# Kernel tuning notes

Hardware: AMD Instinct MI355X
Metric: run time of the kernel (lower is better)

Reference implementation:

```python
import jax, jax.numpy as jnp
import numpy as np

N_TARGETS = 4
BATCH_SIZE = 4
B = N_TARGETS * BATCH_SIZE
N_SAMPLES = 1024
LAYERS = [(128, 128), (256, 64), (512, 32)]  # (channels, spatial)
EPS_COS = 1e-10


def setup_inputs() -> dict:
    key = jax.random.key(0)
    inp = {}
    for l, (c, s) in enumerate(LAYERS):
        k1, k2, k3, k4, key = jax.random.split(key, 5)
        n = s * s
        inp[f't{l}'] = jax.random.normal(k1, (N_TARGETS, c, s, s), dtype=jnp.float32)
        inp[f'g{l}'] = jax.random.normal(k2, (B, c, s, s), dtype=jnp.float32)
        inp[f'ix{l}'] = jax.random.randint(k3, (B, N_SAMPLES), 0, n)
        inp[f'iy{l}'] = jax.random.randint(k4, (B, N_SAMPLES), 0, n)
    return inp


def _cos_remd(x, y):
    # x: (b,n,c), y: (b,m,c)
    xn = jnp.linalg.norm(x, axis=2, keepdims=True)            # (b,n,1)
    yn = jnp.linalg.norm(y, axis=2, keepdims=True)            # (b,m,1)
    cross = jnp.einsum('bnc,bmc->bnm', x, y)                  # (b,n,m)
    dist = 1.0 - cross / (xn * yn.transpose(0, 2, 1) + EPS_COS)
    m1 = dist.min(axis=1).mean(axis=1)                        # min over n, mean over m
    m2 = dist.min(axis=2).mean(axis=1)                        # min over m, mean over n
    return jnp.maximum(m1, m2)                                # (b,)


def _moment_loss(x, y):
    mu_x = x.mean(axis=1, keepdims=True)
    mu_y = y.mean(axis=1, keepdims=True)
    mu_diff = jnp.abs(mu_x - mu_y).mean(axis=(1, 2))
    x_c = x - mu_x
    y_c = y - mu_y
    x_cov = jnp.einsum('bnc,bnd->bcd', x_c, x_c) / (x.shape[1] - 1)
    y_cov = jnp.einsum('bmc,bmd->bcd', y_c, y_c) / (y.shape[1] - 1)
    cov_diff = jnp.abs(x_cov - y_cov).mean(axis=(1, 2))
    return mu_diff + cov_diff                                 # (b,)


def _layer_loss(t, g, ix, iy):
    b, c, h, w = g.shape
    y = jnp.tile(t, (BATCH_SIZE, 1, 1, 1)).reshape(b, t.shape[1], -1)  # (b,c,n_y)
    x = g.reshape(b, c, -1)                                            # (b,c,n_x)
    x = jnp.take_along_axis(x, ix[:, None, :], axis=2)                 # (b,c,ns)
    y = jnp.take_along_axis(y, iy[:, None, :], axis=2)                 # (b,c,ns)
    x = x.transpose(0, 2, 1)
    y = y.transpose(0, 2, 1)
    return _cos_remd(x, y) + _moment_loss(x, y)


def reference(t0, g0, t1, g1, t2, g2, ix0, iy0, ix1, iy1, ix2, iy2):
    loss = (_layer_loss(t0, g0, ix0, iy0)
            + _layer_loss(t1, g1, ix1, iy1)
            + _layer_loss(t2, g2, ix2, iy2))
    return loss.reshape(BATCH_SIZE, N_TARGETS).mean(axis=0)   # (n_targets,)
```

## Files before the change

### kernel.cpp

```cpp
#include <hip/hip_runtime.h>
#include <math.h>

#define NT 4
#define BSZ 4
#define BB 16
#define NS 1024
#define CHF 1024
#define MAXL 3

typedef unsigned short u16;
typedef __attribute__((ext_vector_type(8))) short bf16x8;
typedef __attribute__((ext_vector_type(4))) float f32x4;

struct LayerP {
    const float *g, *t;
    const int *ix, *iy;
    u16 *Xt, *Yt, *Xs, *Ys;
    float *xp, *yp;
    float *psx, *psy;
    float *rxn, *ryn;
    float *sx, *sy;
    unsigned *m1u, *m2u;
    float *cov;
    int C, n, nchunk, ntri, lid, hs, csl, xblk, yblk;
};
struct Tab {
    LayerP L[MAXL];
    int nl, nb, b0, ysh;
    float* losspart;
};

__device__ __forceinline__ unsigned fenc(float f) {
    unsigned u = __float_as_uint(f);
    return (u & 0x80000000u) ? ~u : (u | 0x80000000u);
}
__device__ __forceinline__ float fdec(unsigned u) {
    unsigned v = (u & 0x80000000u) ? (u & 0x7FFFFFFFu) : ~u;
    return __uint_as_float(v);
}
__device__ __forceinline__ u16 f2bf(float f) {
    unsigned u = __float_as_uint(f);
    unsigned r = u + 0x7FFFu + ((u >> 16) & 1u);
    return (u16)(r >> 16);
}
__device__ __forceinline__ float bf2f(u16 h) {
    return __uint_as_float((unsigned)h << 16);
}

__device__ __forceinline__ void gload16(const float* src, float* dst) {
    __builtin_amdgcn_global_load_lds(
        (const __attribute__((address_space(1))) float*)src,
        (__attribute__((address_space(3))) float*)dst, 16, 0, 0);
}
__device__ __forceinline__ void wait_rem(int rem) {
    if (rem >= 3)      asm volatile("s_waitcnt vmcnt(3)" ::: "memory");
    else if (rem == 2) asm volatile("s_waitcnt vmcnt(2)" ::: "memory");
    else if (rem == 1) asm volatile("s_waitcnt vmcnt(1)" ::: "memory");
    else               asm volatile("s_waitcnt vmcnt(0)" ::: "memory");
}

__global__ __launch_bounds__(256) void gather(Tab tab)
{
    int f = blockIdx.x;
    int l = 0, side = 0, c = 0, grp = 0, h = 0;
    #pragma unroll
    for (int li = 0; li < MAXL; ++li) {
        if (li >= tab.nl) break;
        if (f < tab.L[li].xblk) { l = li; side = 0; goto decoded; }
        f -= tab.L[li].xblk;
        if (f < tab.L[li].yblk) { l = li; side = 1; goto decoded; }
        f -= tab.L[li].yblk;
    }
decoded:;
    const LayerP P = tab.L[l];
    c = f % P.C; f /= P.C;
    int ytg = (tab.ysh == NT) ? NT : tab.nb;
    int gdim = side ? ytg : tab.nb;
    grp = f % gdim; h = f / gdim;

    int tid = threadIdx.x;
    int wv = tid >> 6, lane = tid & 63;
    int csl = P.csl;
    int sbase = h * csl * CHF;
    __shared__ __align__(16) float buf[4][CHF];
    __shared__ float red[4][4];

    if (side == 0) {
        int bl = grp, bg = tab.b0 + bl;
        const float* __restrict__ grow = P.g + ((size_t)bg * P.C + c) * P.n;
        const int* __restrict__ ixr = P.ix + bg * NS;
        int px[4];
        #pragma unroll
        for (int r = 0; r < 4; ++r) px[r] = ixr[tid + r * 256] - sbase;
        __builtin_amdgcn_sched_barrier(0);
        for (int d = 0; d < csl; ++d)
            gload16(grow + sbase + d * CHF + wv * 256 + lane * 4, &buf[d][wv * 256]);
        float xv[4] = {0.f, 0.f, 0.f, 0.f};
        for (int ch = 0; ch < csl; ++ch) {
            wait_rem(csl - 1 - ch);
            __builtin_amdgcn_s_barrier();
            __builtin_amdgcn_sched_barrier(0);
            #pragma unroll
            for (int r = 0; r < 4; ++r) {
                int rel = px[r] - ch * CHF;
                if ((unsigned)rel < (unsigned)CHF) xv[r] = buf[ch][rel];
            }
        }
        u16* __restrict__ xo = P.Xt + ((size_t)bl * P.C + c) * NS;
        float ax = 0.f;
        #pragma unroll
        for (int r = 0; r < 4; ++r) {
            if ((unsigned)px[r] < (unsigned)(csl * CHF)) {
                u16 hb = f2bf(xv[r]);
                xo[tid + r * 256] = hb;
                ax += bf2f(hb);
            }
        }
        for (int o = 32; o > 0; o >>= 1) ax += __shfl_down(ax, o);
        if (lane == 0) red[0][wv] = ax;
        __syncthreads();
        if (tid == 0)
            P.psx[((size_t)h * tab.nb + bl) * P.C + c] =
                red[0][0] + red[0][1] + red[0][2] + red[0][3];
    } else {
        int nk, tgt, bls[4];
        if (tab.ysh == NT) {
            nk = 4; tgt = grp;
            #pragma unroll
            for (int k = 0; k < 4; ++k) bls[k] = tgt + NT * k;
        } else {
            nk = 1; bls[0] = grp; tgt = (tab.b0 + grp) % NT;
            bls[1] = bls[2] = bls[3] = 0;
        }
        const float* __restrict__ trow = P.t + ((size_t)tgt * P.C + c) * P.n;
        int py[4][4];
        #pragma unroll
        for (int k = 0; k < 4; ++k)
            if (k < nk) {
                const int* iyr = P.iy + (tab.b0 + bls[k]) * NS;
                #pragma unroll
                for (int r = 0; r < 4; ++r) py[k][r] = iyr[tid + r * 256] - sbase;
            }
        __builtin_amdgcn_sched_barrier(0);
        for (int d = 0; d < csl; ++d)
            gload16(trow + sbase + d * CHF + wv * 256 + lane * 4, &buf[d][wv * 256]);
        float yv[4][4];
        #pragma unroll
        for (int k = 0; k < 4; ++k)
            #pragma unroll
            for (int r = 0; r < 4; ++r) yv[k][r] = 0.f;
        for (int ch = 0; ch < csl; ++ch) {
            wait_rem(csl - 1 - ch);
            __builtin_amdgcn_s_barrier();
            __builtin_amdgcn_sched_barrier(0);
            #pragma unroll
            for (int k = 0; k < 4; ++k)
                if (k < nk) {
                    #pragma unroll
                    for (int r = 0; r < 4; ++r) {
                        int rel = py[k][r] - ch * CHF;
                        if ((unsigned)rel < (unsigned)CHF) yv[k][r] = buf[ch][rel];
                    }
                }
        }
        #pragma unroll
        for (int k = 0; k < 4; ++k) {
            if (k >= nk) break;
            u16* __restrict__ yo = P.Yt + ((size_t)bls[k] * P.C + c) * NS;
            float ay = 0.f;
            #pragma unroll
            for (int r = 0; r < 4; ++r) {
                if ((unsigned)py[k][r] < (unsigned)(csl * CHF)) {
                    u16 hb = f2bf(yv[k][r]);
                    yo[tid + r * 256] = hb;
                    ay += bf2f(hb);
                }
            }
            for (int o = 32; o > 0; o >>= 1) ay += __shfl_down(ay, o);
            if (lane == 0) red[k][wv] = ay;
        }
        __syncthreads();
        if (tid < nk)
            P.psy[((size_t)h * tab.nb + bls[tid]) * P.C + c] =
                red[tid][0] + red[tid][1] + red[tid][2] + red[tid][3];
    }
}

__global__ void transpose_k(Tab tab)
{
    int x = blockIdx.x, l = 0;
    while (l < MAXL - 1 && x >= tab.L[l].C / 64) { x -= tab.L[l].C / 64; ++l; }
    const LayerP P = tab.L[l];
    int z = blockIdx.z;
    int bl = z >> 1, which = z & 1;
    const u16* __restrict__ Zt = which ? P.Yt : P.Xt;
    u16* __restrict__ Zs = which ? P.Ys : P.Xs;
    float* __restrict__ zp = which ? P.yp : P.xp;
    int C = P.C;
    int ctile = x;
    int c0 = ctile * 64, s0 = blockIdx.y * 64;
    __shared__ __align__(16) u16 T[64][72];
    int tid = threadIdx.x;
    #pragma unroll
    for (int rep = 0; rep < 2; ++rep) {
        int q = tid + rep * 256;
        int rr = q >> 3, seg = q & 7;
        *(float4*)&T[rr][seg * 8] =
            *(const float4*)&Zt[((size_t)bl * C + c0 + rr) * NS + s0 + seg * 8];
    }
    __syncthreads();
    #pragma unroll
    for (int rep = 0; rep < 2; ++rep) {
        int q = tid + rep * 256;
        int sr = q >> 3, cs = q & 7;
        __align__(16) u16 tmp[8];
        float p = 0.f;
        #pragma unroll
        for (int e = 0; e < 8; ++e) {
            u16 h = T[cs * 8 + e][sr];
            tmp[e] = h;
            float v = bf2f(h);
            p = fmaf(v, v, p);
        }
        *(float4*)&Zs[((size_t)bl * NS + s0 + sr) * C + c0 + cs * 8] = *(float4*)tmp;
        p += __shfl_xor(p, 1);
        p += __shfl_xor(p, 2);
        p += __shfl_xor(p, 4);
        if (cs == 0)
            zp[((size_t)bl * P.nchunk + ctile) * NS + s0 + sr] = p;
    }
}

__global__ void colnorm_reduce(Tab tab)
{
    const LayerP P = tab.L[blockIdx.y];
    int bl = blockIdx.z;
    int nb = tab.nb;
    int s = blockIdx.x * 256 + threadIdx.x;
    float ax = 0.f, ay = 0.f;
    for (int k = 0; k < P.nchunk; ++k) {
        size_t o = ((size_t)bl * P.nchunk + k) * NS + s;
        ax += P.xp[o];
        ay += P.yp[o];
    }
    P.rxn[bl * NS + s] = rsqrtf(ax);
    P.ryn[bl * NS + s] = rsqrtf(ay);
    P.m1u[bl * NS + s] = 0xFFFFFFFFu;
    P.m2u[bl * NS + s] = 0xFFFFFFFFu;
    int cq = P.C >> 2;
    for (int c = blockIdx.x * cq + threadIdx.x; c < (blockIdx.x + 1) * cq; c += 256) {
        float sx = 0.f, sy = 0.f;
        for (int h = 0; h < P.hs; ++h) {
            sx += P.psx[((size_t)h * nb + bl) * P.C + c];
            sy += P.psy[((size_t)h * nb + bl) * P.C + c];
        }
        P.sx[bl * P.C + c] = sx;
        P.sy[bl * P.C + c] = sy;
    }
}

__global__ __launch_bounds__(256) void cross_mfma(Tab tab)
{
    int z = blockIdx.z;
    int l = z / tab.nb, bl = z - l * tab.nb;
    const LayerP P = tab.L[l];
    int C = P.C;
    int i0 = blockIdx.x * 128, j0 = blockIdx.y * 128;
    __shared__ __align__(16) u16 As[128][40], Bs[128][40];
    int tid = threadIdx.x;
    int w = tid >> 6, lane = tid & 63;
    int wr = w >> 1, wc = w & 1;
    int q = lane >> 4, r = lane & 15;
    const u16* __restrict__ Xb = P.Xs + ((size_t)bl * NS + i0) * C;
    const u16* __restrict__ Yb = P.Ys + ((size_t)bl * NS + j0) * C;
    f32x4 acc[4][4];
    #pragma unroll
    for (int m = 0; m < 4; ++m)
        #pragma unroll
        for (int nn = 0; nn < 4; ++nn) acc[m][nn] = (f32x4){0.f, 0.f, 0.f, 0.f};

    for (int kk = 0; kk < C; kk += 32) {
        __syncthreads();
        #pragma unroll
        for (int rep = 0; rep < 2; ++rep) {
            int qid = tid + rep * 256;
            int row = qid >> 2, seg = qid & 3;
            size_t off = (size_t)row * C + kk + seg * 8;
            *(float4*)&As[row][seg * 8] = *(const float4*)&Xb[off];
            *(float4*)&Bs[row][seg * 8] = *(const float4*)&Yb[off];
        }
        __syncthreads();
        bf16x8 a[4], b[4];
        #pragma unroll
        for (int m = 0; m < 4; ++m)
            a[m] = *(const bf16x8*)&As[wr * 64 + m * 16 + r][q * 8];
        #pragma unroll
        for (int nn = 0; nn < 4; ++nn)
            b[nn] = *(const bf16x8*)&Bs[wc * 64 + nn * 16 + r][q * 8];
        #pragma unroll
        for (int m = 0; m < 4; ++m)
            #pragma unroll
            for (int nn = 0; nn < 4; ++nn)
                acc[m][nn] = __builtin_amdgcn_mfma_f32_16x16x32_bf16(a[m], b[nn], acc[m][nn], 0, 0, 0);
    }

    float rxl[4][4], ryl[4];
    #pragma unroll
    for (int m = 0; m < 4; ++m)
        #pragma unroll
        for (int reg = 0; reg < 4; ++reg)
            rxl[m][reg] = P.rxn[bl * NS + i0 + wr * 64 + m * 16 + q * 4 + reg];
    #pragma unroll
    for (int nn = 0; nn < 4; ++nn)
        ryl[nn] = P.ryn[bl * NS + j0 + wc * 64 + nn * 16 + r];

    float rm[4][4], cm[4];
    #pragma unroll
    for (int m = 0; m < 4; ++m)
        #pragma unroll
        for (int reg = 0; reg < 4; ++reg) rm[m][reg] = 1e30f;
    #pragma unroll
    for (int nn = 0; nn < 4; ++nn) cm[nn] = 1e30f;
    #pragma unroll
    for (int m = 0; m < 4; ++m)
        #pragma unroll
        for (int nn = 0; nn < 4; ++nn)
            #pragma unroll
            for (int reg = 0; reg < 4; ++reg) {
                float d = 1.f - acc[m][nn][reg] * rxl[m][reg] * ryl[nn];
                rm[m][reg] = fminf(rm[m][reg], d);
                cm[nn] = fminf(cm[nn], d);
            }
    #pragma unroll
    for (int m = 0; m < 4; ++m)
        #pragma unroll
        for (int reg = 0; reg < 4; ++reg) {
            float v = rm[m][reg];
            v = fminf(v, __shfl_xor(v, 1));
            v = fminf(v, __shfl_xor(v, 2));
            v = fminf(v, __shfl_xor(v, 4));
            v = fminf(v, __shfl_xor(v, 8));
            rm[m][reg] = v;
        }
    if (r == 0) {
        #pragma unroll
        for (int m = 0; m < 4; ++m)
            #pragma unroll
            for (int reg = 0; reg < 4; ++reg) {
                int i = i0 + wr * 64 + m * 16 + q * 4 + reg;
                atomicMin(&P.m2u[bl * NS + i], fenc(rm[m][reg]));
            }
    }
    #pragma unroll
    for (int nn = 0; nn < 4; ++nn) {
        float v = cm[nn];
        v = fminf(v, __shfl_xor(v, 16));
        v = fminf(v, __shfl_xor(v, 32));
        cm[nn] = v;
    }
    if (q == 0) {
        #pragma unroll
        for (int nn = 0; nn < 4; ++nn) {
            int j = j0 + wc * 64 + nn * 16 + r;
            atomicMin(&P.m1u[bl * NS + j], fenc(cm[nn]));
        }
    }
}

__global__ __launch_bounds__(256) void cov_mfma(Tab tab)
{
    int x = blockIdx.x, l = 0;
    while (l < MAXL - 1 && x >= tab.L[l].ntri) { x -= tab.L[l].ntri; ++l; }
    const LayerP P = tab.L[l];
    int u = x;
    int bl = blockIdx.y;
    int C = P.C;
    int ty = 0;
    while ((ty + 1) * (ty + 2) / 2 <= u) ++ty;
    int tx = u - ty * (ty + 1) / 2;
    int c0 = ty * 128, d0 = tx * 128;
    float wgt = (tx == ty) ? 1.f : 2.f;

    __shared__ __align__(16) u16 As[128][40], Bs[128][40], Cs2[128][40], Ds[128][40];
    int tid = threadIdx.x;
    int w = tid >> 6, lane = tid & 63;
    int wr = w >> 1, wc = w & 1;
    int q = lane >> 4, r = lane & 15;
    const u16* __restrict__ Xc = P.Xt + ((size_t)bl * C + c0) * NS;
    const u16* __restrict__ Xd = P.Xt + ((size_t)bl * C + d0) * NS;
    const u16* __restrict__ Yc = P.Yt + ((size_t)bl * C + c0) * NS;
    const u16* __restrict__ Yd = P.Yt + ((size_t)bl * C + d0) * NS;

    f32x4 accX[4][4], accY[4][4];
    #pragma unroll
    for (int m = 0; m < 4; ++m)
        #pragma unroll
        for (int nn = 0; nn < 4; ++nn) {
            accX[m][nn] = (f32x4){0.f, 0.f, 0.f, 0.f};
            accY[m][nn] = (f32x4){0.f, 0.f, 0.f, 0.f};
        }

    for (int ss = 0; ss < NS; ss += 32) {
        __syncthreads();
        #pragma unroll
        for (int rep = 0; rep < 2; ++rep) {
            int qid = tid + rep * 256;
            int row = qid >> 2, seg = qid & 3;
            size_t off = (size_t)row * NS + ss + seg * 8;
            *(float4*)&As[row][seg * 8]  = *(const float4*)&Xc[off];
            *(float4*)&Bs[row][seg * 8]  = *(const float4*)&Xd[off];
            *(float4*)&Cs2[row][seg * 8] = *(const float4*)&Yc[off];
            *(float4*)&Ds[row][seg * 8]  = *(const float4*)&Yd[off];
        }
        __syncthreads();
        {
            bf16x8 a[4], b[4];
            #pragma unroll
            for (int m = 0; m < 4; ++m) a[m] = *(const bf16x8*)&As[wr * 64 + m * 16 + r][q * 8];
            #pragma unroll
            for (int nn = 0; nn < 4; ++nn) b[nn] = *(const bf16x8*)&Bs[wc * 64 + nn * 16 + r][q * 8];
            #pragma unroll
            for (int m = 0; m < 4; ++m)
                #pragma unroll
                for (int nn = 0; nn < 4; ++nn)
                    accX[m][nn] = __builtin_amdgcn_mfma_f32_16x16x32_bf16(a[m], b[nn], accX[m][nn], 0, 0, 0);
        }
        {
            bf16x8 a[4], b[4];
            #pragma unroll
            for (int m = 0; m < 4; ++m) a[m] = *(const bf16x8*)&Cs2[wr * 64 + m * 16 + r][q * 8];
            #pragma unroll
            for (int nn = 0; nn < 4; ++nn) b[nn] = *(const bf16x8*)&Ds[wc * 64 + nn * 16 + r][q * 8];
            #pragma unroll
            for (int m = 0; m < 4; ++m)
                #pragma unroll
                for (int nn = 0; nn < 4; ++nn)
                    accY[m][nn] = __builtin_amdgcn_mfma_f32_16x16x32_bf16(a[m], b[nn], accY[m][nn], 0, 0, 0);
        }
    }

    float scxv[4][4], scyv[4][4], sdxv[4], sdyv[4];
    #pragma unroll
    for (int m = 0; m < 4; ++m)
        #pragma unroll
        for (int reg = 0; reg < 4; ++reg) {
            int c = c0 + wr * 64 + m * 16 + q * 4 + reg;
            scxv[m][reg] = P.sx[bl * C + c];
            scyv[m][reg] = P.sy[bl * C + c];
        }
    #pragma unroll
    for (int nn = 0; nn < 4; ++nn) {
        int d = d0 + wc * 64 + nn * 16 + r;
        sdxv[nn] = P.sx[bl * C + d];
        sdyv[nn] = P.sy[bl * C + d];
    }
    const float invNS = 1.f / NS, invNSm1 = 1.f / (NS - 1);
    float tsum = 0.f;
    #pragma unroll
    for (int m = 0; m < 4; ++m)
        #pragma unroll
        for (int nn = 0; nn < 4; ++nn)
            #pragma unroll
            for (int reg = 0; reg < 4; ++reg) {
                float cx = (accX[m][nn][reg] - scxv[m][reg] * sdxv[nn] * invNS) * invNSm1;
                float cy = (accY[m][nn][reg] - scyv[m][reg] * sdyv[nn] * invNS) * invNSm1;
                tsum += fabsf(cx - cy);
            }
    tsum *= wgt;
    __shared__ float redc[4];
    for (int o = 32; o > 0; o >>= 1) tsum += __shfl_down(tsum, o);
    if (lane == 0) redc[w] = tsum;
    __syncthreads();
    if (tid == 0)
        P.cov[(size_t)bl * P.ntri + u] = redc[0] + redc[1] + redc[2] + redc[3];
}

__global__ void finalize_kernel(Tab tab)
{
    const LayerP P = tab.L[blockIdx.x];
    int bl = blockIdx.y;
    int tid = threadIdx.x;
    int C = P.C;
    float s1 = 0.f, s2 = 0.f, smu = 0.f, scov = 0.f;
    for (int s = tid; s < NS; s += 256) {
        s1 += fdec(P.m1u[bl * NS + s]);
        s2 += fdec(P.m2u[bl * NS + s]);
    }
    for (int c = tid; c < C; c += 256) smu += fabsf(P.sx[bl * C + c] - P.sy[bl * C + c]);
    for (int i = tid; i < P.ntri; i += 256) scov += P.cov[(size_t)bl * P.ntri + i];
    __shared__ float red[4][4];
    for (int o = 32; o > 0; o >>= 1) {
        s1 += __shfl_down(s1, o);
        s2 += __shfl_down(s2, o);
        smu += __shfl_down(smu, o);
        scov += __shfl_down(scov, o);
    }
    int wid = tid >> 6, lane = tid & 63;
    if (lane == 0) { red[0][wid] = s1; red[1][wid] = s2; red[2][wid] = smu; red[3][wid] = scov; }
    __syncthreads();
    if (tid == 0) {
        s1 = red[0][0] + red[0][1] + red[0][2] + red[0][3];
        s2 = red[1][0] + red[1][1] + red[1][2] + red[1][3];
        smu = red[2][0] + red[2][1] + red[2][2] + red[2][3];
        scov = red[3][0] + red[3][1] + red[3][2] + red[3][3];
        float m1m = s1 * (1.f / NS), m2m = s2 * (1.f / NS);
        float mu_diff = smu * (1.f / NS) * (1.f / (float)C);
        float cov_diff = scov / ((float)C * (float)C);
        tab.losspart[(tab.b0 + bl) * 3 + P.lid] = fmaxf(m1m, m2m) + mu_diff + cov_diff;
    }
}

__global__ void out_kernel(const float* __restrict__ lp, float* __restrict__ out)
{
    int t = threadIdx.x;
    if (t < NT) {
        float s = 0.f;
        for (int k = 0; k < BSZ; ++k)
            for (int l = 0; l < 3; ++l)
                s += lp[(k * NT + t) * 3 + l];
        out[t] = s * (1.f / BSZ);
    }
}

static inline size_t alignup(size_t v) { return (v + 255) & ~(size_t)255; }

static void geo(int n, int& hs, int& csl) {
    int nch = n >> 10;
    if (nch < 1) nch = 1;
    hs = (nch >= 4) ? nch / 4 : 1;
    csl = nch / hs;
}

static size_t layer_bytes(int C, int n, int nb) {
    int nchunk = C / 64;
    int tc = C / 128, ntri = tc * (tc + 1) / 2;
    int hs, csl; geo(n, hs, csl);
    size_t szZ = alignup((size_t)NS * C * 2);
    size_t szP = alignup((size_t)nchunk * NS * 4);
    size_t szPS = alignup((size_t)hs * nb * C * 4);
    return (size_t)nb * (4 * szZ + 2 * szP + 4 * alignup(NS * 4)
                         + 2 * alignup(C * 4) + alignup(ntri * 4))
           + 2 * szPS;
}

static char* fill_layer(LayerP& P, char* p, int C, int n, int nb, int ysh, int lid,
                        const float* g, const float* t, const int* ix, const int* iy) {
    P.g = g; P.t = t; P.ix = ix; P.iy = iy;
    P.C = C; P.n = n; P.lid = lid;
    P.nchunk = C / 64;
    int tc = C / 128;
    P.ntri = tc * (tc + 1) / 2;
    geo(n, P.hs, P.csl);
    P.xblk = C * P.hs * nb;
    P.yblk = C * P.hs * ((ysh == NT) ? NT : nb);
    size_t szZ = alignup((size_t)NS * C * 2);
    size_t szP = alignup((size_t)P.nchunk * NS * 4);
    size_t szPS = alignup((size_t)P.hs * nb * C * 4);
    P.Xt = (u16*)p;  p += nb * szZ;
    P.Yt = (u16*)p;  p += nb * szZ;
    P.Xs = (u16*)p;  p += nb * szZ;
    P.Ys = (u16*)p;  p += nb * szZ;
    P.xp = (float*)p; p += nb * szP;
    P.yp = (float*)p; p += nb * szP;
    P.psx = (float*)p; p += szPS;
    P.psy = (float*)p; p += szPS;
    P.rxn = (float*)p; p += nb * alignup(NS * 4);
    P.ryn = (float*)p; p += nb * alignup(NS * 4);
    P.m1u = (unsigned*)p; p += nb * alignup(NS * 4);
    P.m2u = (unsigned*)p; p += nb * alignup(NS * 4);
    P.sx = (float*)p; p += nb * alignup(C * 4);
    P.sy = (float*)p; p += nb * alignup(C * 4);
    P.cov = (float*)p; p += nb * alignup(P.ntri * 4);
    return p;
}

static void launch_group(const Tab& tab, hipStream_t stream) {
    int sumC64 = 0, sumNtri = 0, flatN = 0;
    for (int l = 0; l < tab.nl; ++l) {
        sumC64 += tab.L[l].C / 64;
        sumNtri += tab.L[l].ntri;
        flatN += tab.L[l].xblk + tab.L[l].yblk;
    }
    int nb = tab.nb;
    gather<<<flatN, 256, 0, stream>>>(tab);
    transpose_k<<<dim3(sumC64, NS / 64, nb * 2), 256, 0, stream>>>(tab);
    colnorm_reduce<<<dim3(NS / 256, tab.nl, nb), 256, 0, stream>>>(tab);
    cross_mfma<<<dim3(NS / 128, NS / 128, tab.nl * nb), 256, 0, stream>>>(tab);
    cov_mfma<<<dim3(sumNtri, nb), 256, 0, stream>>>(tab);
    finalize_kernel<<<dim3(tab.nl, nb), 256, 0, stream>>>(tab);
}

extern "C" void kernel_launch(void* const* d_in, const int* in_sizes, int n_in,
                              void* d_out, int out_size, void* d_ws, size_t ws_size,
                              hipStream_t stream)
{
    const float* tp[3] = {(const float*)d_in[0], (const float*)d_in[4], (const float*)d_in[8]};
    const float* gp[3] = {(const float*)d_in[1], (const float*)d_in[5], (const float*)d_in[9]};
    const int* ixp[3]  = {(const int*)d_in[2], (const int*)d_in[6], (const int*)d_in[10]};
    const int* iyp[3]  = {(const int*)d_in[3], (const int*)d_in[7], (const int*)d_in[11]};
    const int Cs[3] = {128, 256, 512};
    const int Sp[3] = {128, 64, 32};

    float* out = (float*)d_out;
    char* ws = (char*)d_ws;
    float* losspart = (float*)ws;
    size_t base = alignup(BB * 3 * 4);
    size_t avail = (ws_size > base) ? ws_size - base : 0;

    size_t need_all = 0;
    for (int l = 0; l < 3; ++l) need_all += layer_bytes(Cs[l], Sp[l] * Sp[l], BB);

    if (avail >= need_all) {
        Tab tab;
        tab.nl = 3; tab.nb = BB; tab.b0 = 0; tab.ysh = NT; tab.losspart = losspart;
        char* p = ws + base;
        for (int l = 0; l < 3; ++l)
            p = fill_layer(tab.L[l], p, Cs[l], Sp[l] * Sp[l], BB, NT, l,
                           gp[l], tp[l], ixp[l], iyp[l]);
        launch_group(tab, stream);
    } else {
        for (int l = 0; l < 3; ++l) {
            size_t per_b = layer_bytes(Cs[l], Sp[l] * Sp[l], 1);
            int G = (int)(avail / per_b);
            if (G > BB) G = BB;
            if (G < 1) G = 1;
            for (int b0 = 0; b0 < BB; b0 += G) {
                int nb = (BB - b0 < G) ? (BB - b0) : G;
                Tab tab;
                tab.nl = 1; tab.nb = nb; tab.b0 = b0; tab.ysh = 1; tab.losspart = losspart;
                fill_layer(tab.L[0], ws + base, Cs[l], Sp[l] * Sp[l], nb, 1, l,
                           gp[l], tp[l], ixp[l], iyp[l]);
                launch_group(tab, stream);
            }
        }
    }
    out_kernel<<<1, 64, 0, stream>>>(losspart, out);
}
```

Before: 228.1 us.

## Gather four channels per block with double-buffered chunk streaming

The gather kernel now handles four channels per block, one wave loading each channel's spatial chunk, instead of one channel per block. Chunks are streamed through a two-stage LDS double buffer with prefetch two steps ahead, replacing the old scheme that loaded all chunks at once. The goal is to amortize the index loads and block launch overhead over more channels and to overlap loads with the gather. In exchange each thread holds more registers (up to 64 floats on the target side), there are four times fewer blocks, and extra barriers are added per step.

Measured after the change: 228.2 us. About the same (+0.1%).

```diff
diff --git a/kernel.cpp b/kernel.cpp
--- a/kernel.cpp
+++ b/kernel.cpp
@@ -5,7 +5,6 @@
 #define BSZ 4
 #define BB 16
 #define NS 1024
-#define CHF 1024
 #define MAXL 3
 
 typedef unsigned short u16;
@@ -52,17 +51,11 @@
         (const __attribute__((address_space(1))) float*)src,
         (__attribute__((address_space(3))) float*)dst, 16, 0, 0);
 }
-__device__ __forceinline__ void wait_rem(int rem) {
-    if (rem >= 3)      asm volatile("s_waitcnt vmcnt(3)" ::: "memory");
-    else if (rem == 2) asm volatile("s_waitcnt vmcnt(2)" ::: "memory");
-    else if (rem == 1) asm volatile("s_waitcnt vmcnt(1)" ::: "memory");
-    else               asm volatile("s_waitcnt vmcnt(0)" ::: "memory");
-}
 
 __global__ __launch_bounds__(256) void gather(Tab tab)
 {
     int f = blockIdx.x;
-    int l = 0, side = 0, c = 0, grp = 0, h = 0;
+    int l = 0, side = 0;
     #pragma unroll
     for (int li = 0; li < MAXL; ++li) {
         if (li >= tab.nl) break;
@@ -73,55 +66,83 @@
     }
 decoded:;
     const LayerP P = tab.L[l];
-    c = f % P.C; f /= P.C;
+    int cg4 = P.C >> 2;
+    int cgi = f % cg4; f /= cg4;
     int ytg = (tab.ysh == NT) ? NT : tab.nb;
     int gdim = side ? ytg : tab.nb;
-    grp = f % gdim; h = f / gdim;
+    int grp = f % gdim;
+    int h = f / gdim;
+    int c0 = cgi * 4;
 
     int tid = threadIdx.x;
-    int wv = tid >> 6, lane = tid & 63;
-    int csl = P.csl;
-    int sbase = h * csl * CHF;
-    __shared__ __align__(16) float buf[4][CHF];
-    __shared__ float red[4][4];
+    int w = tid >> 6, lane = tid & 63;
+    int nsteps = P.csl;
+    int sbase = h * nsteps * 1024;
+    int srange = nsteps * 1024;
+    __shared__ __align__(16) float buf[2][4][1024];
+    __shared__ float red[4][4][4];
 
     if (side == 0) {
         int bl = grp, bg = tab.b0 + bl;
-        const float* __restrict__ grow = P.g + ((size_t)bg * P.C + c) * P.n;
+        const float* __restrict__ grow = P.g + ((size_t)bg * P.C + c0 + w) * P.n;
         const int* __restrict__ ixr = P.ix + bg * NS;
         int px[4];
         #pragma unroll
         for (int r = 0; r < 4; ++r) px[r] = ixr[tid + r * 256] - sbase;
-        __builtin_amdgcn_sched_barrier(0);
-        for (int d = 0; d < csl; ++d)
-            gload16(grow + sbase + d * CHF + wv * 256 + lane * 4, &buf[d][wv * 256]);
-        float xv[4] = {0.f, 0.f, 0.f, 0.f};
-        for (int ch = 0; ch < csl; ++ch) {
-            wait_rem(csl - 1 - ch);
+        int npro = nsteps < 2 ? nsteps : 2;
+        for (int s = 0; s < npro; ++s)
+            #pragma unroll
+            for (int j = 0; j < 4; ++j)
+                gload16(grow + sbase + s * 1024 + j * 256 + lane * 4, &buf[s][w][j * 256]);
+        float xv[4][4];
+        #pragma unroll
+        for (int cc = 0; cc < 4; ++cc)
+            #pragma unroll
+            for (int r = 0; r < 4; ++r) xv[cc][r] = 0.f;
+        for (int s = 0; s < nsteps; ++s) {
+            if (s + 1 < nsteps) asm volatile("s_waitcnt vmcnt(4)" ::: "memory");
+            else                asm volatile("s_waitcnt vmcnt(0)" ::: "memory");
             __builtin_amdgcn_s_barrier();
             __builtin_amdgcn_sched_barrier(0);
+            int lo = s * 1024;
             #pragma unroll
             for (int r = 0; r < 4; ++r) {
-                int rel = px[r] - ch * CHF;
-                if ((unsigned)rel < (unsigned)CHF) xv[r] = buf[ch][rel];
-            }
-        }
-        u16* __restrict__ xo = P.Xt + ((size_t)bl * P.C + c) * NS;
-        float ax = 0.f;
+                int rel = px[r] - lo;
+                if ((unsigned)rel < 1024u) {
+                    #pragma unroll
+                    for (int cc = 0; cc < 4; ++cc) xv[cc][r] = buf[s & 1][cc][rel];
+                }
+            }
+            if (s + 2 < nsteps) {
+                __builtin_amdgcn_s_barrier();
+                #pragma unroll
+                for (int j = 0; j < 4; ++j)
+                    gload16(grow + sbase + (s + 2) * 1024 + j * 256 + lane * 4,
+                            &buf[s & 1][w][j * 256]);
+            }
+        }
+        float ax[4] = {0.f, 0.f, 0.f, 0.f};
         #pragma unroll
         for (int r = 0; r < 4; ++r) {
-            if ((unsigned)px[r] < (unsigned)(csl * CHF)) {
-                u16 hb = f2bf(xv[r]);
-                xo[tid + r * 256] = hb;
-                ax += bf2f(hb);
-            }
-        }
-        for (int o = 32; o > 0; o >>= 1) ax += __shfl_down(ax, o);
-        if (lane == 0) red[0][wv] = ax;
+            if ((unsigned)px[r] < (unsigned)srange) {
+                #pragma unroll
+                for (int cc = 0; cc < 4; ++cc) {
+                    u16 hb = f2bf(xv[cc][r]);
+                    P.Xt[((size_t)bl * P.C + c0 + cc) * NS + tid + r * 256] = hb;
+                    ax[cc] += bf2f(hb);
+                }
+            }
+        }
+        #pragma unroll
+        for (int cc = 0; cc < 4; ++cc) {
+            float v = ax[cc];
+            for (int o = 32; o > 0; o >>= 1) v += __shfl_down(v, o);
+            if (lane == 0) red[0][cc][w] = v;
+        }
         __syncthreads();
-        if (tid == 0)
-            P.psx[((size_t)h * tab.nb + bl) * P.C + c] =
-                red[0][0] + red[0][1] + red[0][2] + red[0][3];
+        if (tid < 4)
+            P.psx[((size_t)h * tab.nb + bl) * P.C + c0 + tid] =
+                red[0][tid][0] + red[0][tid][1] + red[0][tid][2] + red[0][tid][3];
     } else {
         int nk, tgt, bls[4];
         if (tab.ysh == NT) {
@@ -132,7 +153,7 @@
             nk = 1; bls[0] = grp; tgt = (tab.b0 + grp) % NT;
             bls[1] = bls[2] = bls[3] = 0;
         }
-        const float* __restrict__ trow = P.t + ((size_t)tgt * P.C + c) * P.n;
+        const float* __restrict__ trow = P.t + ((size_t)tgt * P.C + c0 + w) * P.n;
         int py[4][4];
         #pragma unroll
         for (int k = 0; k < 4; ++k)
@@ -141,48 +162,72 @@
                 #pragma unroll
                 for (int r = 0; r < 4; ++r) py[k][r] = iyr[tid + r * 256] - sbase;
             }
-        __builtin_amdgcn_sched_barrier(0);
-        for (int d = 0; d < csl; ++d)
-            gload16(trow + sbase + d * CHF + wv * 256 + lane * 4, &buf[d][wv * 256]);
-        float yv[4][4];
-        #pragma unroll
-        for (int k = 0; k < 4; ++k)
-            #pragma unroll
-            for (int r = 0; r < 4; ++r) yv[k][r] = 0.f;
-        for (int ch = 0; ch < csl; ++ch) {
-            wait_rem(csl - 1 - ch);
+        int npro = nsteps < 2 ? nsteps : 2;
+        for (int s = 0; s < npro; ++s)
+            #pragma unroll
+            for (int j = 0; j < 4; ++j)
+                gload16(trow + sbase + s * 1024 + j * 256 + lane * 4, &buf[s][w][j * 256]);
+        float yv[4][4][4];
+        #pragma unroll
+        for (int cc = 0; cc < 4; ++cc)
+            #pragma unroll
+            for (int k = 0; k < 4; ++k)
+                #pragma unroll
+                for (int r = 0; r < 4; ++r) yv[cc][k][r] = 0.f;
+        for (int s = 0; s < nsteps; ++s) {
+            if (s + 1 < nsteps) asm volatile("s_waitcnt vmcnt(4)" ::: "memory");
+            else                asm volatile("s_waitcnt vmcnt(0)" ::: "memory");
             __builtin_amdgcn_s_barrier();
             __builtin_amdgcn_sched_barrier(0);
+            int lo = s * 1024;
             #pragma unroll
             for (int k = 0; k < 4; ++k)
                 if (k < nk) {
                     #pragma unroll
                     for (int r = 0; r < 4; ++r) {
-                        int rel = py[k][r] - ch * CHF;
-                        if ((unsigned)rel < (unsigned)CHF) yv[k][r] = buf[ch][rel];
+                        int rel = py[k][r] - lo;
+                        if ((unsigned)rel < 1024u) {
+                            #pragma unroll
+                            for (int cc = 0; cc < 4; ++cc) yv[cc][k][r] = buf[s & 1][cc][rel];
+                        }
                     }
                 }
+            if (s + 2 < nsteps) {
+                __builtin_amdgcn_s_barrier();
+                #pragma unroll
+                for (int j = 0; j < 4; ++j)
+                    gload16(trow + sbase + (s + 2) * 1024 + j * 256 + lane * 4,
+                            &buf[s & 1][w][j * 256]);
+            }
         }
         #pragma unroll
         for (int k = 0; k < 4; ++k) {
             if (k >= nk) break;
-            u16* __restrict__ yo = P.Yt + ((size_t)bls[k] * P.C + c) * NS;
-            float ay = 0.f;
+            float ay[4] = {0.f, 0.f, 0.f, 0.f};
             #pragma unroll
             for (int r = 0; r < 4; ++r) {
-                if ((unsigned)py[k][r] < (unsigned)(csl * CHF)) {
-                    u16 hb = f2bf(yv[k][r]);
-                    yo[tid + r * 256] = hb;
-                    ay += bf2f(hb);
+                if ((unsigned)py[k][r] < (unsigned)srange) {
+                    #pragma unroll
+                    for (int cc = 0; cc < 4; ++cc) {
+                        u16 hb = f2bf(yv[cc][k][r]);
+                        P.Yt[((size_t)bls[k] * P.C + c0 + cc) * NS + tid + r * 256] = hb;
+                        ay[cc] += bf2f(hb);
+                    }
                 }
             }
-            for (int o = 32; o > 0; o >>= 1) ay += __shfl_down(ay, o);
-            if (lane == 0) red[k][wv] = ay;
+            #pragma unroll
+            for (int cc = 0; cc < 4; ++cc) {
+                float v = ay[cc];
+                for (int o = 32; o > 0; o >>= 1) v += __shfl_down(v, o);
+                if (lane == 0) red[k][cc][w] = v;
+            }
         }
         __syncthreads();
-        if (tid < nk)
-            P.psy[((size_t)h * tab.nb + bls[tid]) * P.C + c] =
-                red[tid][0] + red[tid][1] + red[tid][2] + red[tid][3];
+        if (tid < 4 * nk) {
+            int k = tid >> 2, cc = tid & 3;
+            P.psy[((size_t)h * tab.nb + bls[k]) * P.C + c0 + cc] =
+                red[k][cc][0] + red[k][cc][1] + red[k][cc][2] + red[k][cc][3];
+        }
     }
 }
 
@@ -551,8 +596,8 @@
     int tc = C / 128;
     P.ntri = tc * (tc + 1) / 2;
     geo(n, P.hs, P.csl);
-    P.xblk = C * P.hs * nb;
-    P.yblk = C * P.hs * ((ysh == NT) ? NT : nb);
+    P.xblk = (C / 4) * P.hs * nb;
+    P.yblk = (C / 4) * P.hs * ((ysh == NT) ? NT : nb);
     size_t szZ = alignup((size_t)NS * C * 2);
     size_t szP = alignup((size_t)P.nchunk * NS * 4);
     size_t szPS = alignup((size_t)P.hs * nb * C * 4);
```
